# Performance work log

Measured on AMD Instinct MI355X. Metric: run time of the kernel, lower is better.

Reference implementation:

```python
import jax, jax.numpy as jnp
import numpy as np

EMBED_DIM = 512
NUM_HEAD = 16
HEAD_DIM = EMBED_DIM // NUM_HEAD
EPS = 1e-6


def setup_inputs() -> dict:
    key = jax.random.key(0)
    ks = jax.random.split(key, 7)
    B, L = 4, 4096
    scale = 1.0 / np.sqrt(EMBED_DIM)
    return {
        "query": jax.random.normal(ks[0], (B, L, EMBED_DIM), jnp.float32),
        "key": jax.random.normal(ks[1], (B, L, EMBED_DIM), jnp.float32),
        "value": jax.random.normal(ks[2], (B, L, EMBED_DIM), jnp.float32),
        "Wq": jax.random.normal(ks[3], (EMBED_DIM, EMBED_DIM), jnp.float32) * scale,
        "Wk": jax.random.normal(ks[4], (EMBED_DIM, EMBED_DIM), jnp.float32) * scale,
        "Wv": jax.random.normal(ks[5], (EMBED_DIM, EMBED_DIM), jnp.float32) * scale,
        "Wm": jax.random.normal(ks[6], (EMBED_DIM, EMBED_DIM), jnp.float32) * scale,
    }


def reference(query, key, value, Wq, Wk, Wv, Wm):
    bs, Lq, E = query.shape
    H, D = NUM_HEAD, HEAD_DIM
    # projections (nn.Linear without bias: x @ W.T)
    q = (query @ Wq.T).reshape(bs, Lq, H, D)
    k = (key @ Wk.T).reshape(bs, -1, H, D)
    v = (value @ Wv.T).reshape(bs, -1, H, D)
    # elu+1 feature map
    Q = jax.nn.elu(q) + 1.0
    K = jax.nn.elu(k) + 1.0
    v_len = v.shape[1]
    v = v / v_len
    # KV accumulation: [n, h, d, dv]
    KV = jnp.einsum('nshd,nshv->nhdv', K, v)
    # normalizer Z: [n, l, h]
    Z = 1.0 / (jnp.einsum('nlhd,nhd->nlh', Q, K.sum(axis=1)) + EPS)
    # weighted combination: [n, l, h, dv]
    message = jnp.einsum('nlhd,nhdv,nlh->nlhv', Q, KV, Z) * v_len
    # merge projection (dropout p=0 -> identity)
    out = message.reshape(bs, Lq, H * D) @ Wm.T
    return out
```

## Files before the change

### kernel.cpp

```cpp
#include <hip/hip_runtime.h>

#define EMBED  512
#define NHEAD  16
#define HDIM   32
#define NBATCH 4
#define SEQ    4096
#define NROWS  (NBATCH * SEQ)
#define FEPS   1e-6f

typedef __attribute__((ext_vector_type(8))) short short8;
typedef __attribute__((ext_vector_type(4))) float f32x4;

__device__ __forceinline__ short f2bf(float x) {
    unsigned u = __float_as_uint(x);
    u += 0x7FFFu + ((u >> 16) & 1u);
    return (short)(u >> 16);
}
__device__ __forceinline__ float bf2f(short h) {
    return __uint_as_float(((unsigned)(unsigned short)h) << 16);
}

__global__ __launch_bounds__(256)
void convert_w(const float* __restrict__ W, short* __restrict__ hi,
               short* __restrict__ lo) {
    int i = (blockIdx.x * 256 + threadIdx.x) * 4;
    float4 v = *(const float4*)(W + i);
    short4 h, l;
    h.x = f2bf(v.x); l.x = f2bf(v.x - bf2f(h.x));
    h.y = f2bf(v.y); l.y = f2bf(v.y - bf2f(h.y));
    h.z = f2bf(v.z); l.z = f2bf(v.z - bf2f(h.z));
    h.w = f2bf(v.w); l.w = f2bf(v.w - bf2f(h.w));
    *(short4*)(hi + i) = h;
    *(short4*)(lo + i) = l;
}

#define LDA 40

template <int EPI>
__global__ __launch_bounds__(256, 2)
void gemm_mfma(const float* __restrict__ A, const short* __restrict__ Whi,
               const short* __restrict__ Wlo, float* __restrict__ C) {
    __shared__ short Ah[128][LDA];
    __shared__ short Al[128][LDA];

    const int tid  = threadIdx.x;
    const int lane = tid & 63;
    const int wave = tid >> 6;
    const int wm   = (wave >> 1) * 64;
    const int wn   = (wave & 1) * 64;
    const int l15  = lane & 15;
    const int kg   = lane >> 4;
    const int bm   = blockIdx.y * 128;
    const int bn   = blockIdx.x * 128;

    const int sr = tid >> 2;
    const int sk = (tid & 3) * 8;
    const float* Ap0 = A + (size_t)(bm + sr) * EMBED + sk;
    const float* Ap1 = Ap0 + (size_t)64 * EMBED;

    const short* Bh = Whi + (size_t)(bn + wn + l15) * EMBED + kg * 8;
    const short* Bl = Wlo + (size_t)(bn + wn + l15) * EMBED + kg * 8;

    f32x4 acc[4][4];
#pragma unroll
    for (int i = 0; i < 4; ++i)
#pragma unroll
        for (int j = 0; j < 4; ++j) acc[i][j] = (f32x4)0.0f;

#pragma unroll 1
    for (int k0 = 0; k0 < EMBED; k0 += 32) {
        float4 a0 = *(const float4*)(Ap0 + k0);
        float4 a1 = *(const float4*)(Ap0 + k0 + 4);
        float4 a2 = *(const float4*)(Ap1 + k0);
        float4 a3 = *(const float4*)(Ap1 + k0 + 4);
        short8 bh[4], bl[4];
#pragma unroll
        for (int j = 0; j < 4; ++j) {
            bh[j] = *(const short8*)(Bh + (size_t)j * 16 * EMBED + k0);
            bl[j] = *(const short8*)(Bl + (size_t)j * 16 * EMBED + k0);
        }
        __syncthreads();
        {
            float v[8] = {a0.x, a0.y, a0.z, a0.w, a1.x, a1.y, a1.z, a1.w};
            short8 hv, lv;
#pragma unroll
            for (int i = 0; i < 8; ++i) {
                short hb = f2bf(v[i]);
                hv[i] = hb; lv[i] = f2bf(v[i] - bf2f(hb));
            }
            *(short8*)&Ah[sr][sk] = hv;
            *(short8*)&Al[sr][sk] = lv;
        }
        {
            float v[8] = {a2.x, a2.y, a2.z, a2.w, a3.x, a3.y, a3.z, a3.w};
            short8 hv, lv;
#pragma unroll
            for (int i = 0; i < 8; ++i) {
                short hb = f2bf(v[i]);
                hv[i] = hb; lv[i] = f2bf(v[i] - bf2f(hb));
            }
            *(short8*)&Ah[sr + 64][sk] = hv;
            *(short8*)&Al[sr + 64][sk] = lv;
        }
        __syncthreads();

        short8 ah[4], al[4];
#pragma unroll
        for (int i = 0; i < 4; ++i) {
            ah[i] = *(const short8*)&Ah[wm + i * 16 + l15][kg * 8];
            al[i] = *(const short8*)&Al[wm + i * 16 + l15][kg * 8];
        }
#pragma unroll
        for (int i = 0; i < 4; ++i)
#pragma unroll
            for (int j = 0; j < 4; ++j) {
                acc[i][j] = __builtin_amdgcn_mfma_f32_16x16x32_bf16(ah[i], bh[j], acc[i][j], 0, 0, 0);
                acc[i][j] = __builtin_amdgcn_mfma_f32_16x16x32_bf16(ah[i], bl[j], acc[i][j], 0, 0, 0);
                acc[i][j] = __builtin_amdgcn_mfma_f32_16x16x32_bf16(al[i], bh[j], acc[i][j], 0, 0, 0);
            }
    }

#pragma unroll
    for (int i = 0; i < 4; ++i)
#pragma unroll
        for (int j = 0; j < 4; ++j) {
            const int col = bn + wn + j * 16 + l15;
#pragma unroll
            for (int r = 0; r < 4; ++r) {
                const int row = bm + wm + i * 16 + kg * 4 + r;
                float vv = acc[i][j][r];
                if (EPI == 1) vv = (vv > 0.f) ? (vv + 1.f) : __expf(vv);
                else if (EPI == 2) vv = vv * (1.0f / (float)SEQ);
                C[(size_t)row * EMBED + col] = vv;
            }
        }
}

__global__ __launch_bounds__(256)
void kv_ksum_kernel(const float* __restrict__ Kf, const float* __restrict__ Vf,
                    float* __restrict__ KV, float* __restrict__ Ksum) {
    const int bh = blockIdx.y;
    const int b  = bh >> 4;
    const int h  = bh & 15;
    const int s0 = blockIdx.x * (SEQ / 8);
    const int t  = threadIdx.x;
    const int e  = t & 31;
    const int dg = t >> 5;

    __shared__ float Ks[32][32];
    __shared__ float Vs[32][32];
    const int lr = t >> 3, lc = (t & 7) * 4;

    const float* Kbase = Kf + (size_t)b * SEQ * EMBED + h * HDIM;
    const float* Vbase = Vf + (size_t)b * SEQ * EMBED + h * HDIM;

    float a0 = 0.f, a1 = 0.f, a2 = 0.f, a3 = 0.f, ks = 0.f;
    for (int s = s0; s < s0 + SEQ / 8; s += 32) {
        float4 kx = *(const float4*)(Kbase + (size_t)(s + lr) * EMBED + lc);
        float4 vx = *(const float4*)(Vbase + (size_t)(s + lr) * EMBED + lc);
        __syncthreads();
        *(float4*)&Ks[lr][lc] = kx;
        *(float4*)&Vs[lr][lc] = vx;
        __syncthreads();
#pragma unroll
        for (int rr = 0; rr < 32; ++rr) {
            float v = Vs[rr][e];
            a0 = fmaf(Ks[rr][dg * 4 + 0], v, a0);
            a1 = fmaf(Ks[rr][dg * 4 + 1], v, a1);
            a2 = fmaf(Ks[rr][dg * 4 + 2], v, a2);
            a3 = fmaf(Ks[rr][dg * 4 + 3], v, a3);
            if (dg == 0) ks += Ks[rr][e];
        }
    }
    float* kvp = KV + ((size_t)bh * HDIM + dg * 4) * HDIM + e;
    atomicAdd(kvp + 0 * HDIM, a0);
    atomicAdd(kvp + 1 * HDIM, a1);
    atomicAdd(kvp + 2 * HDIM, a2);
    atomicAdd(kvp + 3 * HDIM, a3);
    if (dg == 0) atomicAdd(&Ksum[bh * HDIM + e], ks);
}

__global__ __launch_bounds__(512)
void message_kernel(float* __restrict__ Q, const float* __restrict__ KV,
                    const float* __restrict__ Ksum) {
    const int blk  = blockIdx.x;
    const int row0 = blk * 4;
    const int b    = row0 >> 12;
    const int t    = threadIdx.x;
    const int h    = t >> 5, e = t & 31;

    __shared__ float q[4][EMBED];
    __shared__ float ks[EMBED];
    ks[t] = Ksum[b * EMBED + t];
#pragma unroll
    for (int r = 0; r < 4; ++r) q[r][t] = Q[(size_t)(row0 + r) * EMBED + t];

    const float* kvh = KV + (size_t)(b * NHEAD + h) * HDIM * HDIM + e;
    float kc[HDIM];
#pragma unroll
    for (int d = 0; d < HDIM; ++d) kc[d] = kvh[d * HDIM];
    __syncthreads();

#pragma unroll
    for (int r = 0; r < 4; ++r) {
        float zden = FEPS, m = 0.f;
#pragma unroll
        for (int d = 0; d < HDIM; ++d) {
            float qd = q[r][h * HDIM + d];
            zden = fmaf(qd, ks[h * HDIM + d], zden);
            m    = fmaf(qd, kc[d], m);
        }
        Q[(size_t)(row0 + r) * EMBED + t] = m * ((float)SEQ / zden);
    }
}

extern "C" void kernel_launch(void* const* d_in, const int* in_sizes, int n_in,
                              void* d_out, int out_size, void* d_ws, size_t ws_size,
                              hipStream_t stream) {
    const float* query = (const float*)d_in[0];
    const float* key   = (const float*)d_in[1];
    const float* value = (const float*)d_in[2];
    const float* Wq    = (const float*)d_in[3];
    const float* Wk    = (const float*)d_in[4];
    const float* Wv    = (const float*)d_in[5];
    const float* Wm    = (const float*)d_in[6];
    float* out = (float*)d_out;

    float* ws  = (float*)d_ws;
    float* Qb  = ws;
    float* Kb  = Qb + (size_t)NROWS * EMBED;
    float* Vb  = Kb + (size_t)NROWS * EMBED;
    float* KVb = Vb + (size_t)NROWS * EMBED;
    float* KSb = KVb + 64 * HDIM * HDIM;
    short* wsp = (short*)(KSb + 64 * HDIM);
    const int WN = EMBED * EMBED;
    short* WqH = wsp;            short* WqL = wsp + WN;
    short* WkH = wsp + 2 * WN;   short* WkL = wsp + 3 * WN;
    short* WvH = wsp + 4 * WN;   short* WvL = wsp + 5 * WN;
    short* WmH = wsp + 6 * WN;   short* WmL = wsp + 7 * WN;

    hipMemsetAsync(KVb, 0, (64 * HDIM * HDIM + 64 * HDIM) * sizeof(float), stream);

    const int cblk = WN / (256 * 4);
    convert_w<<<cblk, 256, 0, stream>>>(Wq, WqH, WqL);
    convert_w<<<cblk, 256, 0, stream>>>(Wk, WkH, WkL);
    convert_w<<<cblk, 256, 0, stream>>>(Wv, WvH, WvL);
    convert_w<<<cblk, 256, 0, stream>>>(Wm, WmH, WmL);

    dim3 g(EMBED / 128, NROWS / 128);
    gemm_mfma<1><<<g, 256, 0, stream>>>(query, WqH, WqL, Qb);
    gemm_mfma<1><<<g, 256, 0, stream>>>(key,   WkH, WkL, Kb);
    gemm_mfma<2><<<g, 256, 0, stream>>>(value, WvH, WvL, Vb);

    kv_ksum_kernel<<<dim3(8, 64), 256, 0, stream>>>(Kb, Vb, KVb, KSb);
    message_kernel<<<NROWS / 4, 512, 0, stream>>>(Qb, KVb, KSb);

    gemm_mfma<0><<<g, 256, 0, stream>>>(Qb, WmH, WmL, out);
}
```

Before: 367.6 us.

## Retile GEMM with prefetch and LDS epilogue, MFMA KV reduction, fused weight conversion

The projection GEMM moves from 128x128 to 128x64 tiles with a linear block index that walks M fastest. It prefetches the next A and B slices into registers, raises the occupancy hint to 3, and stages the output through LDS so rows are written with coalesced float4 stores. The KV/Ksum reduction is rewritten to use split-bf16 MFMA instructions, with a ones vector for the K sum, and the per-wave partials are reduced in LDS before the atomics. The four weight-conversion launches are merged into one. The smaller tile re-reads each A tile twice and the prefetch registers raise register pressure.

```diff
diff --git a/kernel.cpp b/kernel.cpp
--- a/kernel.cpp
+++ b/kernel.cpp
@@ -21,163 +21,270 @@
 }
 
 __global__ __launch_bounds__(256)
-void convert_w(const float* __restrict__ W, short* __restrict__ hi,
-               short* __restrict__ lo) {
-    int i = (blockIdx.x * 256 + threadIdx.x) * 4;
+void convert_w4(const float* __restrict__ W0, const float* __restrict__ W1,
+                const float* __restrict__ W2, const float* __restrict__ W3,
+                short* __restrict__ H0, short* __restrict__ L0,
+                short* __restrict__ H1, short* __restrict__ L1,
+                short* __restrict__ H2, short* __restrict__ L2,
+                short* __restrict__ H3, short* __restrict__ L3) {
+    const int seg = blockIdx.x >> 8;
+    const int i = ((blockIdx.x & 255) * 256 + threadIdx.x) * 4;
+    const float* W = (seg == 0) ? W0 : (seg == 1) ? W1 : (seg == 2) ? W2 : W3;
+    short* H = (seg == 0) ? H0 : (seg == 1) ? H1 : (seg == 2) ? H2 : H3;
+    short* L = (seg == 0) ? L0 : (seg == 1) ? L1 : (seg == 2) ? L2 : L3;
     float4 v = *(const float4*)(W + i);
     short4 h, l;
     h.x = f2bf(v.x); l.x = f2bf(v.x - bf2f(h.x));
     h.y = f2bf(v.y); l.y = f2bf(v.y - bf2f(h.y));
     h.z = f2bf(v.z); l.z = f2bf(v.z - bf2f(h.z));
     h.w = f2bf(v.w); l.w = f2bf(v.w - bf2f(h.w));
-    *(short4*)(hi + i) = h;
-    *(short4*)(lo + i) = l;
+    *(short4*)(H + i) = h;
+    *(short4*)(L + i) = l;
 }
 
 #define LDA 40
 
 template <int EPI>
-__global__ __launch_bounds__(256, 2)
+__global__ __launch_bounds__(256, 3)
 void gemm_mfma(const float* __restrict__ A, const short* __restrict__ Whi,
                const short* __restrict__ Wlo, float* __restrict__ C) {
-    __shared__ short Ah[128][LDA];
-    __shared__ short Al[128][LDA];
+    __shared__ char smem[34048];
+    short (*Ah)[LDA] = (short (*)[LDA])smem;
+    short (*Al)[LDA] = (short (*)[LDA])(smem + 10240);
 
     const int tid  = threadIdx.x;
     const int lane = tid & 63;
     const int wave = tid >> 6;
-    const int wm   = (wave >> 1) * 64;
-    const int wn   = (wave & 1) * 64;
+    const int wm   = wave * 32;
     const int l15  = lane & 15;
     const int kg   = lane >> 4;
-    const int bm   = blockIdx.y * 128;
-    const int bn   = blockIdx.x * 128;
-
-    const int sr = tid >> 2;
-    const int sk = (tid & 3) * 8;
-    const float* Ap0 = A + (size_t)(bm + sr) * EMBED + sk;
-    const float* Ap1 = Ap0 + (size_t)64 * EMBED;
-
-    const short* Bh = Whi + (size_t)(bn + wn + l15) * EMBED + kg * 8;
-    const short* Bl = Wlo + (size_t)(bn + wn + l15) * EMBED + kg * 8;
-
-    f32x4 acc[4][4];
-#pragma unroll
-    for (int i = 0; i < 4; ++i)
+
+    const int lin = blockIdx.x;
+    const int bn  = (lin >> 7) * 64;
+    const int bm  = (lin & 127) * 128;
+
+    const int sr = tid >> 1;
+    const int sk = (tid & 1) * 16;
+    const float* Ap = A + (size_t)(bm + sr) * EMBED + sk;
+
+    const short* Bh = Whi + (size_t)(bn + l15) * EMBED + kg * 8;
+    const short* Bl = Wlo + (size_t)(bn + l15) * EMBED + kg * 8;
+
+    f32x4 acc[2][4];
+#pragma unroll
+    for (int i = 0; i < 2; ++i)
 #pragma unroll
         for (int j = 0; j < 4; ++j) acc[i][j] = (f32x4)0.0f;
+
+    float4 a[4];
+    short8 bh[4], bl[4], bhn[4], bln[4];
+#pragma unroll
+    for (int p = 0; p < 4; ++p) a[p] = *(const float4*)(Ap + p * 4);
+#pragma unroll
+    for (int j = 0; j < 4; ++j) {
+        bh[j] = *(const short8*)(Bh + (size_t)j * 16 * EMBED);
+        bl[j] = *(const short8*)(Bl + (size_t)j * 16 * EMBED);
+    }
 
 #pragma unroll 1
     for (int k0 = 0; k0 < EMBED; k0 += 32) {
-        float4 a0 = *(const float4*)(Ap0 + k0);
-        float4 a1 = *(const float4*)(Ap0 + k0 + 4);
-        float4 a2 = *(const float4*)(Ap1 + k0);
-        float4 a3 = *(const float4*)(Ap1 + k0 + 4);
-        short8 bh[4], bl[4];
-#pragma unroll
-        for (int j = 0; j < 4; ++j) {
-            bh[j] = *(const short8*)(Bh + (size_t)j * 16 * EMBED + k0);
-            bl[j] = *(const short8*)(Bl + (size_t)j * 16 * EMBED + k0);
-        }
         __syncthreads();
         {
-            float v[8] = {a0.x, a0.y, a0.z, a0.w, a1.x, a1.y, a1.z, a1.w};
-            short8 hv, lv;
-#pragma unroll
-            for (int i = 0; i < 8; ++i) {
-                short hb = f2bf(v[i]);
-                hv[i] = hb; lv[i] = f2bf(v[i] - bf2f(hb));
-            }
-            *(short8*)&Ah[sr][sk] = hv;
-            *(short8*)&Al[sr][sk] = lv;
-        }
-        {
-            float v[8] = {a2.x, a2.y, a2.z, a2.w, a3.x, a3.y, a3.z, a3.w};
-            short8 hv, lv;
-#pragma unroll
-            for (int i = 0; i < 8; ++i) {
-                short hb = f2bf(v[i]);
-                hv[i] = hb; lv[i] = f2bf(v[i] - bf2f(hb));
-            }
-            *(short8*)&Ah[sr + 64][sk] = hv;
-            *(short8*)&Al[sr + 64][sk] = lv;
+            float v[16] = {a[0].x, a[0].y, a[0].z, a[0].w,
+                           a[1].x, a[1].y, a[1].z, a[1].w,
+                           a[2].x, a[2].y, a[2].z, a[2].w,
+                           a[3].x, a[3].y, a[3].z, a[3].w};
+            short8 hv0, lv0, hv1, lv1;
+#pragma unroll
+            for (int q = 0; q < 8; ++q) {
+                short hb = f2bf(v[q]);
+                hv0[q] = hb; lv0[q] = f2bf(v[q] - bf2f(hb));
+            }
+#pragma unroll
+            for (int q = 0; q < 8; ++q) {
+                short hb = f2bf(v[8 + q]);
+                hv1[q] = hb; lv1[q] = f2bf(v[8 + q] - bf2f(hb));
+            }
+            *(short8*)&Ah[sr][sk]     = hv0;
+            *(short8*)&Ah[sr][sk + 8] = hv1;
+            *(short8*)&Al[sr][sk]     = lv0;
+            *(short8*)&Al[sr][sk + 8] = lv1;
         }
         __syncthreads();
 
-        short8 ah[4], al[4];
-#pragma unroll
-        for (int i = 0; i < 4; ++i) {
-            ah[i] = *(const short8*)&Ah[wm + i * 16 + l15][kg * 8];
-            al[i] = *(const short8*)&Al[wm + i * 16 + l15][kg * 8];
-        }
-#pragma unroll
-        for (int i = 0; i < 4; ++i)
+        if (k0 + 32 < EMBED) {
+#pragma unroll
+            for (int p = 0; p < 4; ++p)
+                a[p] = *(const float4*)(Ap + k0 + 32 + p * 4);
 #pragma unroll
             for (int j = 0; j < 4; ++j) {
-                acc[i][j] = __builtin_amdgcn_mfma_f32_16x16x32_bf16(ah[i], bh[j], acc[i][j], 0, 0, 0);
-                acc[i][j] = __builtin_amdgcn_mfma_f32_16x16x32_bf16(ah[i], bl[j], acc[i][j], 0, 0, 0);
-                acc[i][j] = __builtin_amdgcn_mfma_f32_16x16x32_bf16(al[i], bh[j], acc[i][j], 0, 0, 0);
-            }
-    }
-
-#pragma unroll
-    for (int i = 0; i < 4; ++i)
-#pragma unroll
-        for (int j = 0; j < 4; ++j) {
-            const int col = bn + wn + j * 16 + l15;
+                bhn[j] = *(const short8*)(Bh + (size_t)j * 16 * EMBED + k0 + 32);
+                bln[j] = *(const short8*)(Bl + (size_t)j * 16 * EMBED + k0 + 32);
+            }
+        }
+
+        short8 ah[2], alr[2];
+#pragma unroll
+        for (int i = 0; i < 2; ++i) {
+            ah[i]  = *(const short8*)&Ah[wm + i * 16 + l15][kg * 8];
+            alr[i] = *(const short8*)&Al[wm + i * 16 + l15][kg * 8];
+        }
+#pragma unroll
+        for (int i = 0; i < 2; ++i)
+#pragma unroll
+            for (int j = 0; j < 4; ++j) {
+                acc[i][j] = __builtin_amdgcn_mfma_f32_16x16x32_bf16(ah[i],  bh[j], acc[i][j], 0, 0, 0);
+                acc[i][j] = __builtin_amdgcn_mfma_f32_16x16x32_bf16(ah[i],  bl[j], acc[i][j], 0, 0, 0);
+                acc[i][j] = __builtin_amdgcn_mfma_f32_16x16x32_bf16(alr[i], bh[j], acc[i][j], 0, 0, 0);
+            }
+#pragma unroll
+        for (int j = 0; j < 4; ++j) { bh[j] = bhn[j]; bl[j] = bln[j]; }
+    }
+
+    __syncthreads();
+    float* Cw = (float*)smem + wave * 2112;
+#pragma unroll
+    for (int i = 0; i < 2; ++i)
+#pragma unroll
+        for (int j = 0; j < 4; ++j)
 #pragma unroll
             for (int r = 0; r < 4; ++r) {
-                const int row = bm + wm + i * 16 + kg * 4 + r;
                 float vv = acc[i][j][r];
                 if (EPI == 1) vv = (vv > 0.f) ? (vv + 1.f) : __expf(vv);
                 else if (EPI == 2) vv = vv * (1.0f / (float)SEQ);
-                C[(size_t)row * EMBED + col] = vv;
-            }
-        }
+                Cw[(i * 16 + kg * 4 + r) * 66 + j * 16 + l15] = vv;
+            }
+#pragma unroll
+    for (int inst = 0; inst < 8; ++inst) {
+        f32x4 cv = *(const f32x4*)&Cw[(inst * 4 + kg) * 66 + l15 * 4];
+        const int row = bm + wm + inst * 4 + kg;
+        *(float4*)(C + (size_t)row * EMBED + bn + l15 * 4) = *(float4*)&cv;
+    }
 }
 
 __global__ __launch_bounds__(256)
-void kv_ksum_kernel(const float* __restrict__ Kf, const float* __restrict__ Vf,
-                    float* __restrict__ KV, float* __restrict__ Ksum) {
-    const int bh = blockIdx.y;
-    const int b  = bh >> 4;
-    const int h  = bh & 15;
-    const int s0 = blockIdx.x * (SEQ / 8);
-    const int t  = threadIdx.x;
-    const int e  = t & 31;
-    const int dg = t >> 5;
-
-    __shared__ float Ks[32][32];
-    __shared__ float Vs[32][32];
-    const int lr = t >> 3, lc = (t & 7) * 4;
-
+void kv_ksum_mfma(const float* __restrict__ Kf, const float* __restrict__ Vf,
+                  float* __restrict__ KV, float* __restrict__ Ksum) {
+    __shared__ char smem[34816];
+    short (*Kh)[34] = (short (*)[34])smem;
+    short (*Kl)[34] = (short (*)[34])(smem + 8704);
+    short (*Vh)[34] = (short (*)[34])(smem + 17408);
+    short (*Vl)[34] = (short (*)[34])(smem + 26112);
+
+    const int bh_ = blockIdx.y;
+    const int b = bh_ >> 4, h = bh_ & 15;
+    const int s0 = blockIdx.x * 256;
+    const int t = threadIdx.x;
+    const int lane = t & 63, wave = t >> 6;
+    const int l15 = lane & 15, kg = lane >> 4;
+    const int ws = wave * 32;
+
+    const int sl = t >> 1;
+    const int dsel = (t & 1) * 16;
     const float* Kbase = Kf + (size_t)b * SEQ * EMBED + h * HDIM;
     const float* Vbase = Vf + (size_t)b * SEQ * EMBED + h * HDIM;
 
-    float a0 = 0.f, a1 = 0.f, a2 = 0.f, a3 = 0.f, ks = 0.f;
-    for (int s = s0; s < s0 + SEQ / 8; s += 32) {
-        float4 kx = *(const float4*)(Kbase + (size_t)(s + lr) * EMBED + lc);
-        float4 vx = *(const float4*)(Vbase + (size_t)(s + lr) * EMBED + lc);
+    f32x4 kvacc[2][2], ksacc[2];
+#pragma unroll
+    for (int i = 0; i < 2; ++i) {
+        ksacc[i] = (f32x4)0.0f;
+#pragma unroll
+        for (int j = 0; j < 2; ++j) kvacc[i][j] = (f32x4)0.0f;
+    }
+    short8 ones;
+#pragma unroll
+    for (int q = 0; q < 8; ++q) ones[q] = (short)0x3F80;
+
+    float4 kx[4], vx[4];
+#pragma unroll
+    for (int p = 0; p < 4; ++p) {
+        kx[p] = *(const float4*)(Kbase + (size_t)(s0 + sl) * EMBED + dsel + 4 * p);
+        vx[p] = *(const float4*)(Vbase + (size_t)(s0 + sl) * EMBED + dsel + 4 * p);
+    }
+
+#pragma unroll 1
+    for (int it = 0; it < 2; ++it) {
         __syncthreads();
-        *(float4*)&Ks[lr][lc] = kx;
-        *(float4*)&Vs[lr][lc] = vx;
+        {
+            float kv_[8] = {kx[0].x, kx[0].y, kx[0].z, kx[0].w, kx[1].x, kx[1].y, kx[1].z, kx[1].w};
+            float kv2[8] = {kx[2].x, kx[2].y, kx[2].z, kx[2].w, kx[3].x, kx[3].y, kx[3].z, kx[3].w};
+            float vv_[8] = {vx[0].x, vx[0].y, vx[0].z, vx[0].w, vx[1].x, vx[1].y, vx[1].z, vx[1].w};
+            float vv2[8] = {vx[2].x, vx[2].y, vx[2].z, vx[2].w, vx[3].x, vx[3].y, vx[3].z, vx[3].w};
+            short8 h0, l0, h1, l1;
+#pragma unroll
+            for (int q = 0; q < 8; ++q) { short hb = f2bf(kv_[q]); h0[q] = hb; l0[q] = f2bf(kv_[q] - bf2f(hb)); }
+#pragma unroll
+            for (int q = 0; q < 8; ++q) { short hb = f2bf(kv2[q]); h1[q] = hb; l1[q] = f2bf(kv2[q] - bf2f(hb)); }
+            *(short8*)&Kh[sl][dsel] = h0; *(short8*)&Kh[sl][dsel + 8] = h1;
+            *(short8*)&Kl[sl][dsel] = l0; *(short8*)&Kl[sl][dsel + 8] = l1;
+#pragma unroll
+            for (int q = 0; q < 8; ++q) { short hb = f2bf(vv_[q]); h0[q] = hb; l0[q] = f2bf(vv_[q] - bf2f(hb)); }
+#pragma unroll
+            for (int q = 0; q < 8; ++q) { short hb = f2bf(vv2[q]); h1[q] = hb; l1[q] = f2bf(vv2[q] - bf2f(hb)); }
+            *(short8*)&Vh[sl][dsel] = h0; *(short8*)&Vh[sl][dsel + 8] = h1;
+            *(short8*)&Vl[sl][dsel] = l0; *(short8*)&Vl[sl][dsel + 8] = l1;
+        }
         __syncthreads();
-#pragma unroll
-        for (int rr = 0; rr < 32; ++rr) {
-            float v = Vs[rr][e];
-            a0 = fmaf(Ks[rr][dg * 4 + 0], v, a0);
-            a1 = fmaf(Ks[rr][dg * 4 + 1], v, a1);
-            a2 = fmaf(Ks[rr][dg * 4 + 2], v, a2);
-            a3 = fmaf(Ks[rr][dg * 4 + 3], v, a3);
-            if (dg == 0) ks += Ks[rr][e];
-        }
-    }
-    float* kvp = KV + ((size_t)bh * HDIM + dg * 4) * HDIM + e;
-    atomicAdd(kvp + 0 * HDIM, a0);
-    atomicAdd(kvp + 1 * HDIM, a1);
-    atomicAdd(kvp + 2 * HDIM, a2);
-    atomicAdd(kvp + 3 * HDIM, a3);
-    if (dg == 0) atomicAdd(&Ksum[bh * HDIM + e], ks);
+        if (it == 0) {
+#pragma unroll
+            for (int p = 0; p < 4; ++p) {
+                kx[p] = *(const float4*)(Kbase + (size_t)(s0 + 128 + sl) * EMBED + dsel + 4 * p);
+                vx[p] = *(const float4*)(Vbase + (size_t)(s0 + 128 + sl) * EMBED + dsel + 4 * p);
+            }
+        }
+        short8 kah[2], kal[2], vbh[2], vbl[2];
+#pragma unroll
+        for (int i = 0; i < 2; ++i) {
+#pragma unroll
+            for (int q = 0; q < 8; ++q) {
+                const int srow = ws + kg * 8 + q;
+                const int col  = i * 16 + l15;
+                kah[i][q] = Kh[srow][col];
+                kal[i][q] = Kl[srow][col];
+                vbh[i][q] = Vh[srow][col];
+                vbl[i][q] = Vl[srow][col];
+            }
+        }
+#pragma unroll
+        for (int i = 0; i < 2; ++i) {
+#pragma unroll
+            for (int j = 0; j < 2; ++j) {
+                kvacc[i][j] = __builtin_amdgcn_mfma_f32_16x16x32_bf16(kah[i], vbh[j], kvacc[i][j], 0, 0, 0);
+                kvacc[i][j] = __builtin_amdgcn_mfma_f32_16x16x32_bf16(kah[i], vbl[j], kvacc[i][j], 0, 0, 0);
+                kvacc[i][j] = __builtin_amdgcn_mfma_f32_16x16x32_bf16(kal[i], vbh[j], kvacc[i][j], 0, 0, 0);
+            }
+            ksacc[i] = __builtin_amdgcn_mfma_f32_16x16x32_bf16(kah[i], ones, ksacc[i], 0, 0, 0);
+            ksacc[i] = __builtin_amdgcn_mfma_f32_16x16x32_bf16(kal[i], ones, ksacc[i], 0, 0, 0);
+        }
+    }
+
+    __syncthreads();
+    float* red = (float*)smem;
+    float* myred = red + wave * 1056;
+#pragma unroll
+    for (int i = 0; i < 2; ++i)
+#pragma unroll
+        for (int j = 0; j < 2; ++j)
+#pragma unroll
+            for (int r = 0; r < 4; ++r)
+                myred[(i * 16 + kg * 4 + r) * 32 + j * 16 + l15] = kvacc[i][j][r];
+    if (l15 == 0) {
+#pragma unroll
+        for (int i = 0; i < 2; ++i)
+#pragma unroll
+            for (int r = 0; r < 4; ++r)
+                myred[1024 + i * 16 + kg * 4 + r] = ksacc[i][r];
+    }
+    __syncthreads();
+    float* kvout = KV + (size_t)bh_ * 1024;
+    for (int idx = t; idx < 1024; idx += 256) {
+        float s4 = red[idx] + red[1056 + idx] + red[2112 + idx] + red[3168 + idx];
+        atomicAdd(&kvout[idx], s4);
+    }
+    if (t < 32) {
+        float s4 = red[1024 + t] + red[1056 + 1024 + t] + red[2112 + 1024 + t] + red[3168 + 1024 + t];
+        atomicAdd(&Ksum[bh_ * 32 + t], s4);
+    }
 }
 
 __global__ __launch_bounds__(512)
@@ -241,19 +348,16 @@
 
     hipMemsetAsync(KVb, 0, (64 * HDIM * HDIM + 64 * HDIM) * sizeof(float), stream);
 
-    const int cblk = WN / (256 * 4);
-    convert_w<<<cblk, 256, 0, stream>>>(Wq, WqH, WqL);
-    convert_w<<<cblk, 256, 0, stream>>>(Wk, WkH, WkL);
-    convert_w<<<cblk, 256, 0, stream>>>(Wv, WvH, WvL);
-    convert_w<<<cblk, 256, 0, stream>>>(Wm, WmH, WmL);
-
-    dim3 g(EMBED / 128, NROWS / 128);
-    gemm_mfma<1><<<g, 256, 0, stream>>>(query, WqH, WqL, Qb);
-    gemm_mfma<1><<<g, 256, 0, stream>>>(key,   WkH, WkL, Kb);
-    gemm_mfma<2><<<g, 256, 0, stream>>>(value, WvH, WvL, Vb);
-
-    kv_ksum_kernel<<<dim3(8, 64), 256, 0, stream>>>(Kb, Vb, KVb, KSb);
+    convert_w4<<<1024, 256, 0, stream>>>(Wq, Wk, Wv, Wm,
+                                         WqH, WqL, WkH, WkL,
+                                         WvH, WvL, WmH, WmL);
+
+    gemm_mfma<1><<<1024, 256, 0, stream>>>(query, WqH, WqL, Qb);
+    gemm_mfma<1><<<1024, 256, 0, stream>>>(key,   WkH, WkL, Kb);
+    gemm_mfma<2><<<1024, 256, 0, stream>>>(value, WvH, WvL, Vb);
+
+    kv_ksum_mfma<<<dim3(16, 64), 256, 0, stream>>>(Kb, Vb, KVb, KSb);
     message_kernel<<<NROWS / 4, 512, 0, stream>>>(Qb, KVb, KSb);
 
-    gemm_mfma<0><<<g, 256, 0, stream>>>(Qb, WmH, WmL, out);
-}
+    gemm_mfma<0><<<1024, 256, 0, stream>>>(Qb, WmH, WmL, out);
+}
```

Result: slower. 494.1 us (+34.4%).
